# Optimization experiments

Hardware: AMD Instinct MI355X
Metric: run time of the kernel (lower is better)

## Reference

```python
import jax, jax.numpy as jnp
import numpy as np

V, N, D, R, L, KS = 32000, 2048, 1024, 16, 4, 7
B, H = 2, 4 * 1024
GMIN, GMAX, ACAP = 0.85, 1.0, 1.0


def rmsnorm(x, w, eps=1e-6):
    return x * jax.lax.rsqrt(jnp.mean(x * x, axis=-1, keepdims=True) + eps) * w


def l2norm(x, eps=1e-8):
    return x / jnp.maximum(jnp.linalg.norm(x, axis=-1, keepdims=True), eps)


def mlp(x, w1, b1, w2, b2):
    return jax.nn.gelu(x @ w1 + b1) @ w2 + b2


def k1_block(h, nw, w1, b1, w2, b2):
    return h + mlp(rmsnorm(h, nw), w1, b1, w2, b2)


def causal_conv(h, kernel):
    # depthwise causal conv with shared 1D kernel; kernel[0] = current step
    n = h.shape[1]
    hp = jnp.pad(h, ((0, 0), (KS - 1, 0), (0, 0)))
    out = jnp.zeros_like(h)
    for k in range(KS):  # KS is small & static
        out = out + kernel[k] * hp[:, KS - 1 - k: KS - 1 - k + n, :]
    return out


def k2_layer(h, p):
    (u, v, dlog, alog, glog, kern, pw, pb, n1w, n2w, w1, b1, w2, b2) = p
    residual = h
    hn = rmsnorm(h, n1w)
    gate = jax.nn.sigmoid(glog)
    out = gate * causal_conv(hn, kern)
    # low-rank q/k
    q = l2norm(hn @ u)          # (B,N,R)
    k = l2norm(hn @ v)          # (B,N,R)
    gamma = GMIN + (GMAX - GMIN) * jax.nn.sigmoid(dlog)   # (R,)
    alpha = ACAP * jax.nn.sigmoid(alog)                   # (R,)
    qa = q * alpha
    pos = jnp.arange(h.shape[1])
    diff = jnp.maximum(pos[:, None] - pos[None, :], 0).astype(h.dtype)
    mask = (pos[:, None] >= pos[None, :]).astype(h.dtype)
    # per-rank causal decay matrix gamma_r^(i-j): (R,N,N)
    decay = jnp.exp(diff[None] * jnp.log(gamma)[:, None, None]) * mask[None]
    scores = jnp.einsum('bir,rij,bjr->bij', qa, decay, k)  # (B,N,N)
    out = out + jnp.einsum('bij,bjd->bid', scores, hn)
    out = out @ pw + pb
    h = residual + out
    h = h + mlp(rmsnorm(h, n2w), w1, b1, w2, b2)
    return h


def setup_inputs() -> dict:
    key = jax.random.key(0)
    ks = jax.random.split(key, 32)
    f32 = jnp.float32
    inp = {
        'tokens': jax.random.randint(ks[0], (B, N), 0, V),
        'emb_table': jax.random.normal(ks[1], (V, D), f32) * 0.02,
        'k1a_nw': jnp.ones((D,), f32),
        'k1a_w1': jax.random.normal(ks[2], (D, H), f32) * 0.02,
        'k1a_b1': jnp.zeros((H,), f32),
        'k1a_w2': jax.random.normal(ks[3], (H, D), f32) * 0.02,
        'k1a_b2': jnp.zeros((D,), f32),
        'k2_u': jax.random.normal(ks[4], (L, D, R), f32) * 0.05,
        'k2_v': jax.random.normal(ks[5], (L, D, R), f32) * 0.05,
        'k2_dlog': jax.random.normal(ks[6], (L, R), f32) * 0.5,
        'k2_alog': jnp.zeros((L, R), f32),
        'k2_glog': jnp.zeros((L,), f32),
        'k2_kern': jax.random.normal(ks[7], (L, KS), f32) * 0.1,
        'k2_pw': jax.random.normal(ks[8], (L, D, D), f32) * 0.02,
        'k2_pb': jnp.zeros((L, D), f32),
        'k2_n1w': jnp.ones((L, D), f32),
        'k2_n2w': jnp.ones((L, D), f32),
        'k2_w1': jax.random.normal(ks[9], (L, D, H), f32) * 0.02,
        'k2_b1': jnp.zeros((L, H), f32),
        'k2_w2': jax.random.normal(ks[10], (L, H, D), f32) * 0.02,
        'k2_b2': jnp.zeros((L, D), f32),
        'k1b_nw': jnp.ones((D,), f32),
        'k1b_w1': jax.random.normal(ks[11], (D, H), f32) * 0.02,
        'k1b_b1': jnp.zeros((H,), f32),
        'k1b_w2': jax.random.normal(ks[12], (H, D), f32) * 0.02,
        'k1b_b2': jnp.zeros((D,), f32),
        'k0_nw': jnp.ones((D,), f32),
        'head_w': jax.random.normal(ks[13], (D, V), f32) * 0.02,
        'head_b': jnp.zeros((V,), f32),
    }
    return inp


def reference(tokens, emb_table,
              k1a_nw, k1a_w1, k1a_b1, k1a_w2, k1a_b2,
              k2_u, k2_v, k2_dlog, k2_alog, k2_glog, k2_kern,
              k2_pw, k2_pb, k2_n1w, k2_n2w, k2_w1, k2_b1, k2_w2, k2_b2,
              k1b_nw, k1b_w1, k1b_b1, k1b_w2, k1b_b2,
              k0_nw, head_w, head_b):
    h = emb_table[tokens]                                  # (B,N,D)
    h = k1_block(h, k1a_nw, k1a_w1, k1a_b1, k1a_w2, k1a_b2)
    stacked = (k2_u, k2_v, k2_dlog, k2_alog, k2_glog, k2_kern,
               k2_pw, k2_pb, k2_n1w, k2_n2w, k2_w1, k2_b1, k2_w2, k2_b2)
    def step(c, p):
        return k2_layer(c, p), None
    h, _ = jax.lax.scan(step, h, stacked)
    h = k1_block(h, k1b_nw, k1b_w1, k1b_b1, k1b_w2, k1b_b2)
    h = rmsnorm(h, k0_nw)                                  # K0 final norm
    return h @ head_w + head_b                             # (B,N,V)
```

## Files before the change

kernel.cpp:

```cpp
#include <hip/hip_runtime.h>
#include <hip/hip_bf16.h>

#define SEQ 2048
#define DIM 1024
#define RNK 16
#define NL 4
#define KT 7
#define BATCH 2
#define HID 4096
#define VOC 32000
#define BNROWS (BATCH*SEQ)
#define CHK 128
#define NCH (SEQ/CHK)
#define PRMS 128
#define KAPP 160

typedef __hip_bfloat16 bf16;
typedef __attribute__((ext_vector_type(8))) short bh8;
typedef __attribute__((ext_vector_type(4))) float vf4;

__device__ __forceinline__ float bfu(unsigned int u) { u <<= 16; return __builtin_bit_cast(float, u); }
__device__ __forceinline__ unsigned short f2bu(float x) { bf16 t = __float2bfloat16(x); return __builtin_bit_cast(unsigned short, t); }
__device__ __forceinline__ float b2f(bf16 x) { return __bfloat162float(x); }
__device__ __forceinline__ float sigm(float x) { return 1.f / (1.f + expf(-x)); }
__device__ __forceinline__ float gelu_t(float x) {
    float u = 0.7978845608028654f * (x + 0.044715f * x * x * x);
    return 0.5f * x * (1.f + tanhf(u));
}

__device__ __forceinline__ void gld16(const bf16* g, bf16* l) {
    __builtin_amdgcn_global_load_lds(
        (const __attribute__((address_space(1))) void*)g,
        (__attribute__((address_space(3))) void*)l,
        16, 0, 0);
}

__global__ void embed_kernel(const int* __restrict__ tokens, const float* __restrict__ emb,
                             float* __restrict__ h) {
    int row = blockIdx.x;
    int tok = tokens[row];
    const float4* src = (const float4*)(emb + (size_t)tok * DIM);
    float4* dst = (float4*)(h + (size_t)row * DIM);
    dst[threadIdx.x] = src[threadIdx.x];
}

__global__ void rmsnorm_kernel(const float* __restrict__ in, const float* __restrict__ wt,
                               bf16* __restrict__ out) {
    int row = blockIdx.x;
    int tx = threadIdx.x;
    float4 v = ((const float4*)(in + (size_t)row * DIM))[tx];
    float ss = v.x * v.x + v.y * v.y + v.z * v.z + v.w * v.w;
#pragma unroll
    for (int off = 32; off > 0; off >>= 1) ss += __shfl_down(ss, off);
    __shared__ float red[4];
    int lane = tx & 63, wv = tx >> 6;
    if (lane == 0) red[wv] = ss;
    __syncthreads();
    float tot = red[0] + red[1] + red[2] + red[3];
    float scale = rsqrtf(tot * (1.f / DIM) + 1e-6f);
    float4 w4 = ((const float4*)wt)[tx];
    uint2 o;
    o.x = f2bu(v.x * scale * w4.x) | ((unsigned int)f2bu(v.y * scale * w4.y) << 16);
    o.y = f2bu(v.z * scale * w4.z) | ((unsigned int)f2bu(v.w * scale * w4.w) << 16);
    *(uint2*)(out + (size_t)row * DIM + tx * 4) = o;
}

__global__ void transpose_cast_kernel(const float* __restrict__ in, bf16* __restrict__ out,
                                      int K, int Nc) {
    __shared__ float tile[32][33];
    int n0 = blockIdx.x * 32, k0 = blockIdx.y * 32;
    int tx = threadIdx.x & 31, ty = threadIdx.x >> 5;
#pragma unroll
    for (int i = 0; i < 32; i += 8)
        tile[ty + i][tx] = in[(size_t)(k0 + ty + i) * Nc + n0 + tx];
    __syncthreads();
#pragma unroll
    for (int i = 0; i < 32; i += 8)
        out[(size_t)(n0 + ty + i) * K + k0 + tx] = __float2bfloat16(tile[tx][ty + i]);
}

__global__ void prep_kernel(const float* __restrict__ dlog, const float* __restrict__ alog,
                            const float* __restrict__ glog, const float* __restrict__ kern,
                            float* __restrict__ prm) {
    int l = blockIdx.x, t = threadIdx.x;
    float* p = prm + l * PRMS;
    if (t < RNK) {
        float g = 0.85f + 0.15f * sigm(dlog[l * RNK + t]);
        float lg = logf(g);
        p[t] = g;
        p[16 + t] = lg;
        p[32 + t] = expf(lg * (float)CHK);
        p[48 + t] = sigm(alog[l * RNK + t]);
    }
    if (t < KT) {
        float gate = sigm(glog[l]);
        p[64 + t] = gate * kern[l * KT + t];
    }
}

__global__ void prep_uv_kernel(const float* __restrict__ u, const float* __restrict__ v,
                               bf16* __restrict__ uvT) {
    int l = blockIdx.y;
    int k = blockIdx.x * 256 + threadIdx.x;
    const float* ul = u + (size_t)l * DIM * RNK;
    const float* vl = v + (size_t)l * DIM * RNK;
    bf16* o = uvT + (size_t)l * 32 * DIM;
#pragma unroll
    for (int r = 0; r < RNK; ++r) {
        o[(size_t)r * DIM + k] = __float2bfloat16(ul[(size_t)k * RNK + r]);
        o[(size_t)(RNK + r) * DIM + k] = __float2bfloat16(vl[(size_t)k * RNK + r]);
    }
}

__global__ void conv_kernel(const bf16* __restrict__ hn, const float* __restrict__ prm,
                            float* __restrict__ Z) {
    int t = blockIdx.x * 256 + threadIdx.x;
    int d4 = (t & 255) * 4;
    int row = t >> 8;
    int n = row & (SEQ - 1);
    float a0 = 0, a1 = 0, a2 = 0, a3 = 0;
#pragma unroll
    for (int kk = 0; kk < KT; ++kk) {
        if (n - kk < 0) break;
        float wv = prm[64 + kk];
        uint2 hv = *(const uint2*)(hn + (size_t)(row - kk) * DIM + d4);
        a0 += wv * bfu(hv.x & 0xffffu);
        a1 += wv * bfu(hv.x >> 16);
        a2 += wv * bfu(hv.y & 0xffffu);
        a3 += wv * bfu(hv.y >> 16);
    }
    float4 o = {a0, a1, a2, a3};
    *(float4*)(Z + (size_t)row * DIM + d4) = o;
}

__global__ __launch_bounds__(64)
void qk_mfma_kernel(const bf16* __restrict__ hn, const bf16* __restrict__ uvT,
                    const float* __restrict__ prm, float* __restrict__ qa,
                    float* __restrict__ kn) {
    int row0 = blockIdx.x * 16;
    int lane = threadIdx.x;
    int fr = lane & 15, kf = (lane >> 4) * 8;
    vf4 accq = {}, acck = {};
#pragma unroll 4
    for (int kt = 0; kt < DIM / 32; ++kt) {
        int k0 = kt * 32;
        bh8 b0 = *(const bh8*)(uvT + (size_t)fr * DIM + k0 + kf);
        bh8 b1 = *(const bh8*)(uvT + (size_t)(16 + fr) * DIM + k0 + kf);
        bh8 a0 = *(const bh8*)(hn + (size_t)(row0 + fr) * DIM + k0 + kf);
        accq = __builtin_amdgcn_mfma_f32_16x16x32_bf16(a0, b0, accq, 0, 0, 0);
        acck = __builtin_amdgcn_mfma_f32_16x16x32_bf16(a0, b1, acck, 0, 0, 0);
    }
    int fq = lane >> 4;
    float alpha = prm[48 + fr];
#pragma unroll
    for (int j = 0; j < 4; ++j) {
        float qv = accq[j], kv = acck[j];
        float sq = qv * qv, sk = kv * kv;
#pragma unroll
        for (int mask = 1; mask < 16; mask <<= 1) {
            sq += __shfl_xor(sq, mask);
            sk += __shfl_xor(sk, mask);
        }
        int row = row0 + fq * 4 + j;
        qa[(size_t)row * RNK + fr] = qv / fmaxf(sqrtf(sq), 1e-8f) * alpha;
        kn[(size_t)row * RNK + fr] = kv / fmaxf(sqrtf(sk), 1e-8f);
    }
}

__global__ void trans_hn_kernel(const bf16* __restrict__ hn, bf16* __restrict__ HB) {
    __shared__ bf16 tile[32][40];
    int bc = blockIdx.x;
    int d0 = blockIdx.y * 32, j0 = blockIdx.z * 32;
    int tx = threadIdx.x & 31, ty = threadIdx.x >> 5;
    size_t rowb = (size_t)bc * CHK;
#pragma unroll
    for (int i = 0; i < 32; i += 8)
        tile[ty + i][tx] = hn[(rowb + j0 + ty + i) * DIM + d0 + tx];
    __syncthreads();
    bf16* Hp = HB + (size_t)bc * DIM * KAPP;
#pragma unroll
    for (int i = 0; i < 32; i += 8)
        Hp[(size_t)(d0 + ty + i) * KAPP + j0 + tx] = tile[tx][ty + i];
}

__global__ void scores_kernel(const float* __restrict__ qa, const float* __restrict__ kn,
                              const float* __restrict__ prm, bf16* __restrict__ SA,
                              bf16* __restrict__ kdtB) {
    int bc = blockIdx.x;
    int yt = blockIdx.y;
    __shared__ float ptab[CHK][16];
    for (int e = threadIdx.x; e < CHK * 16; e += 256) {
        int tt = e >> 4, r = e & 15;
        ptab[tt][r] = expf(prm[16 + r] * (float)tt);
    }
    __syncthreads();
    size_t rowb = (size_t)bc * CHK;
    bf16* SAp = SA + (size_t)bc * CHK * KAPP;
    for (int e = threadIdx.x; e < 16 * CHK; e += 256) {
        int i = yt * 16 + (e >> 7), j = e & (CHK - 1);
        float vsum = 0.f;
        if (i >= j) {
            const float* qp = qa + (rowb + i) * RNK;
            const float* kp = kn + (rowb + j) * RNK;
#pragma unroll
            for (int r = 0; r < 16; ++r) vsum += qp[r] * ptab[i - j][r] * kp[r];
        }
        SAp[(size_t)i * KAPP + j] = __float2bfloat16(vsum);
    }
    for (int e = threadIdx.x; e < 16 * 32; e += 256) {
        int i = yt * 16 + (e >> 5), rr = e & 31;
        float w = 0.f;
        if (rr < 16) w = qa[(rowb + i) * RNK + rr] * expf(prm[16 + rr] * (float)(i + 1));
        SAp[(size_t)i * KAPP + CHK + rr] = __float2bfloat16(w);
    }
    bf16* kp2 = kdtB + (size_t)bc * RNK * CHK;
    for (int e = threadIdx.x; e < 2 * CHK; e += 256) {
        int r = 2 * yt + (e >> 7), j = e & (CHK - 1);
        kp2[(size_t)r * CHK + j] =
            __float2bfloat16(ptab[CHK - 1 - j][r] * kn[(rowb + j) * RNK + r]);
    }
}

__global__ __launch_bounds__(64)
void chunkU_kernel(const bf16* __restrict__ HB, const bf16* __restrict__ kdtB,
                   float* __restrict__ U) {
    int bc = blockIdx.x;
    int d0 = blockIdx.y * 64;
    int lane = threadIdx.x;
    int fr = lane & 15, kf = (lane >> 4) * 8;
    const bf16* Hp = HB + (size_t)bc * DIM * KAPP;
    const bf16* Kp = kdtB + (size_t)bc * RNK * CHK;
    vf4 acc[4] = {};
#pragma unroll
    for (int kt = 0; kt < 4; ++kt) {
        int k0 = kt * 32;
        bh8 bb = *(const bh8*)(Kp + (size_t)fr * CHK + k0 + kf);
#pragma unroll
        for (int m = 0; m < 4; ++m) {
            bh8 a = *(const bh8*)(Hp + (size_t)(d0 + m * 16 + fr) * KAPP + k0 + kf);
            acc[m] = __builtin_amdgcn_mfma_f32_16x16x32_bf16(a, bb, acc[m], 0, 0, 0);
        }
    }
    int fq = lane >> 4;
    float* Up = U + (size_t)bc * DIM * RNK;
#pragma unroll
    for (int m = 0; m < 4; ++m)
#pragma unroll
        for (int j = 0; j < 4; ++j)
            Up[(size_t)(d0 + m * 16 + fq * 4 + j) * RNK + fr] = acc[m][j];
}

__global__ void scanP_kernel(const float* __restrict__ U, const float* __restrict__ prm,
                             bf16* __restrict__ HB) {
    int g = blockIdx.x * 256 + threadIdx.x;
    int rq = g & 3;
    int d = (g >> 2) & (DIM - 1);
    int b = g >> 12;
    float gC[4], p[4];
#pragma unroll
    for (int q = 0; q < 4; ++q) { gC[q] = prm[32 + rq * 4 + q]; p[q] = 0.f; }
    for (int c = 0; c < NCH; ++c) {
        int bc = b * NCH + c;
        uint2 pk;
        pk.x = (unsigned int)f2bu(p[0]) | ((unsigned int)f2bu(p[1]) << 16);
        pk.y = (unsigned int)f2bu(p[2]) | ((unsigned int)f2bu(p[3]) << 16);
        *(uint2*)(HB + (size_t)bc * DIM * KAPP + (size_t)d * KAPP + CHK + rq * 4) = pk;
        float4 u4 = *(const float4*)(U + ((size_t)bc * DIM + d) * RNK + rq * 4);
        p[0] = gC[0] * p[0] + u4.x;
        p[1] = gC[1] * p[1] + u4.y;
        p[2] = gC[2] * p[2] + u4.z;
        p[3] = gC[3] * p[3] + u4.w;
    }
}

__global__ __launch_bounds__(256)
void apply_gemm_kernel(const bf16* __restrict__ SA, const bf16* __restrict__ HB,
                       const float* __restrict__ Z, bf16* __restrict__ Zb) {
    __shared__ alignas(16) bf16 As[128][40];
    __shared__ alignas(16) bf16 Bs[128][40];
    int bc = blockIdx.y;
    int colB0 = blockIdx.x * 128;
    int t = threadIdx.x;
    int lane = t & 63, wid = t >> 6;
    int wr = wid >> 1, wc = wid & 1;
    vf4 acc[4][4] = {};
    const bf16* A = SA + (size_t)bc * CHK * KAPP;
    const bf16* BT = HB + (size_t)bc * DIM * KAPP;
    int r1 = t >> 2, ko1 = (t & 3) * 8;
    int fr = lane & 15, kf = (lane >> 4) * 8;
#pragma unroll
    for (int kt = 0; kt < 5; ++kt) {
        int k0 = kt * 32;
        int4 va1 = *(const int4*)(A + (size_t)r1 * KAPP + k0 + ko1);
        int4 va2 = *(const int4*)(A + (size_t)(r1 + 64) * KAPP + k0 + ko1);
        int4 vb1 = *(const int4*)(BT + (size_t)(colB0 + r1) * KAPP + k0 + ko1);
        int4 vb2 = *(const int4*)(BT + (size_t)(colB0 + r1 + 64) * KAPP + k0 + ko1);
        __syncthreads();
        *(int4*)&As[r1][ko1] = va1;
        *(int4*)&As[r1 + 64][ko1] = va2;
        *(int4*)&Bs[r1][ko1] = vb1;
        *(int4*)&Bs[r1 + 64][ko1] = vb2;
        __syncthreads();
        bh8 a[4], bb[4];
#pragma unroll
        for (int m = 0; m < 4; ++m) a[m] = *(const bh8*)&As[wr * 64 + m * 16 + fr][kf];
#pragma unroll
        for (int n = 0; n < 4; ++n) bb[n] = *(const bh8*)&Bs[wc * 64 + n * 16 + fr][kf];
#pragma unroll
        for (int m = 0; m < 4; ++m)
#pragma unroll
            for (int n = 0; n < 4; ++n)
                acc[m][n] = __builtin_amdgcn_mfma_f32_16x16x32_bf16(a[m], bb[n], acc[m][n], 0, 0, 0);
    }
    int fq = lane >> 4;
    size_t rowb = (size_t)bc * CHK;
#pragma unroll
    for (int m = 0; m < 4; ++m) {
#pragma unroll
        for (int n = 0; n < 4; ++n) {
            int col = colB0 + wc * 64 + n * 16 + fr;
#pragma unroll
            for (int j = 0; j < 4; ++j) {
                size_t row = rowb + wr * 64 + m * 16 + fq * 4 + j;
                size_t idx = row * DIM + col;
                Zb[idx] = __float2bfloat16(Z[idx] + acc[m][n][j]);
            }
        }
    }
}

template <int EPI>
__global__ __launch_bounds__(256)
void gemm_kernel(const bf16* __restrict__ A, const bf16* __restrict__ BT,
                 const float* __restrict__ bias, const float* __restrict__ res,
                 float* __restrict__ outF, bf16* __restrict__ outB,
                 int M, int Nc, int K, int lda) {
    __shared__ alignas(16) bf16 As[128][32];
    __shared__ alignas(16) bf16 Bs[128][32];
    int gx = gridDim.x;
    int orig = blockIdx.y * gx + blockIdx.x;
    int qch = (gx * gridDim.y) >> 3;
    int wg = (orig & 7) * qch + (orig >> 3);
    int bn = wg % gx, bm = wg / gx;
    int t = threadIdx.x;
    int lane = t & 63, wid = t >> 6;
    int wr = wid >> 1, wc = wid & 1;
    vf4 acc[4][4] = {};
    const int rowA0 = bm * 128, colB0 = bn * 128;
    int fr = lane & 15, kf = (lane >> 4) * 8;
    int c0 = wid * 2;
    int lrow = lane >> 2;
    int lcol = (lane & 3) * 8;
    const bf16* Ag0 = A + (size_t)(rowA0 + c0 * 16 + lrow) * lda + lcol;
    const bf16* Ag1 = A + (size_t)(rowA0 + c0 * 16 + 16 + lrow) * lda + lcol;
    const bf16* Bg0 = BT + (size_t)(colB0 + c0 * 16 + lrow) * lda + lcol;
    const bf16* Bg1 = BT + (size_t)(colB0 + c0 * 16 + 16 + lrow) * lda + lcol;
    bf16* Al0 = &As[0][0] + c0 * 512;
    bf16* Al1 = Al0 + 512;
    bf16* Bl0 = &Bs[0][0] + c0 * 512;
    bf16* Bl1 = Bl0 + 512;
    int nk = K >> 5;
    for (int kt = 0; kt < nk; ++kt) {
        int k0 = kt * 32;
        __syncthreads();
        gld16(Ag0 + k0, Al0);
        gld16(Ag1 + k0, Al1);
        gld16(Bg0 + k0, Bl0);
        gld16(Bg1 + k0, Bl1);
        asm volatile("s_waitcnt vmcnt(0)" ::: "memory");
        __syncthreads();
        bh8 a[4], bb[4];
#pragma unroll
        for (int m = 0; m < 4; ++m) a[m] = *(const bh8*)&As[wr * 64 + m * 16 + fr][kf];
#pragma unroll
        for (int n = 0; n < 4; ++n) bb[n] = *(const bh8*)&Bs[wc * 64 + n * 16 + fr][kf];
#pragma unroll
        for (int m = 0; m < 4; ++m)
#pragma unroll
            for (int n = 0; n < 4; ++n)
                acc[m][n] = __builtin_amdgcn_mfma_f32_16x16x32_bf16(a[m], bb[n], acc[m][n], 0, 0, 0);
    }
    int fq = lane >> 4;
#pragma unroll
    for (int m = 0; m < 4; ++m) {
#pragma unroll
        for (int n = 0; n < 4; ++n) {
            int col = colB0 + wc * 64 + n * 16 + fr;
            float bv = bias[col];
#pragma unroll
            for (int j = 0; j < 4; ++j) {
                int row = rowA0 + wr * 64 + m * 16 + fq * 4 + j;
                size_t idx = (size_t)row * Nc + col;
                float v2 = acc[m][n][j] + bv;
                if (EPI == 1) v2 += res[idx];
                outF[idx] = v2;
            }
        }
    }
}

#define SB __builtin_amdgcn_sched_barrier(0)
template <int EPI>
__global__ __launch_bounds__(512, 2)
void gemm256_kernel(const bf16* __restrict__ A, const bf16* __restrict__ BT,
                    const float* __restrict__ bias,
                    float* __restrict__ outF, bf16* __restrict__ outB,
                    int M, int Nc, int K, int lda) {
    extern __shared__ char smem[];
    bf16* Alds = (bf16*)smem;
    bf16* Blds = (bf16*)(smem + 65536);
    if (EPI == 4) {
        size_t zo = (size_t)blockIdx.z * K;
        A += zo; BT += zo;
        outB += (size_t)blockIdx.z * ((size_t)M * Nc);
    }
    int gx = gridDim.x, gy = gridDim.y;
    int orig = blockIdx.y * gx + blockIdx.x;
    int qch = (gx * gy) >> 3;
    int wg = (orig & 7) * qch + (orig >> 3);
    int bm = wg % gy, bn = wg / gy;
    int rowA0 = bm * 256, colB0 = bn * 256;
    int tid = threadIdx.x;
    int lane = tid & 63, wid = tid >> 6;
    int wm = wid >> 2, wn = wid & 3;
    int fr = lane & 15;
    int kf8 = ((((lane >> 4) & 3) ^ ((fr >> 1) & 3)) * 8);
    int srow = wid * 16 + (lane >> 2);
    int scol = (((lane & 3) ^ ((lane >> 3) & 3)) * 8);
    const bf16* Ags = A + (size_t)(rowA0 + srow) * lda + scol;
    const bf16* Bgs = BT + (size_t)(colB0 + srow) * lda + scol;
    int sbase = wid * 512;
    auto stA = [&](int d, int kh, int k0) {
        bf16* dst = Alds + (d * 2 + kh) * 8192 + sbase;
        const bf16* src = Ags + k0 + kh * 32;
        gld16(src, dst);
        gld16(src + (size_t)128 * lda, dst + 4096);
    };
    auto stB = [&](int d, int kh, int k0) {
        bf16* dst = Blds + (d * 2 + kh) * 8192 + sbase;
        const bf16* src = Bgs + k0 + kh * 32;
        gld16(src, dst);
        gld16(src + (size_t)128 * lda, dst + 4096);
    };
    const bf16* Ard = Alds + (size_t)(wm * 128 + fr) * 32 + kf8;
    const bf16* Brd = Blds + (size_t)(wn * 64 + fr) * 32 + kf8;
    vf4 acc[8][4] = {};
    int nt = K >> 6;
    stA(0, 0, 0); stB(0, 0, 0); stA(0, 1, 0); stB(0, 1, 0);
    for (int t = 0; t < nt; ++t) {
        int d = t & 1, nd = d ^ 1;
        int k1 = (t + 1) << 6;
        bool pf = (t + 1 < nt);
        int dof = d * 16384;
        bh8 bF[4];
        if (pf) { stA(nd, 0, k1); asm volatile("s_waitcnt vmcnt(6)" ::: "memory"); }
        else    {                 asm volatile("s_waitcnt vmcnt(4)" ::: "memory"); }
        SB; __builtin_amdgcn_s_barrier(); SB;
        {
            bh8 a0 = *(const bh8*)(Ard + dof + 0 * 512);
            bh8 a1 = *(const bh8*)(Ard + dof + 1 * 512);
            bh8 a2 = *(const bh8*)(Ard + dof + 2 * 512);
            bh8 a3 = *(const bh8*)(Ard + dof + 3 * 512);
#pragma unroll
            for (int n = 0; n < 4; ++n) bF[n] = *(const bh8*)(Brd + dof + n * 512);
            __builtin_amdgcn_s_setprio(1);
#pragma unroll
            for (int n = 0; n < 4; ++n) {
                acc[0][n] = __builtin_amdgcn_mfma_f32_16x16x32_bf16(a0, bF[n], acc[0][n], 0, 0, 0);
                acc[1][n] = __builtin_amdgcn_mfma_f32_16x16x32_bf16(a1, bF[n], acc[1][n], 0, 0, 0);
                acc[2][n] = __builtin_amdgcn_mfma_f32_16x16x32_bf16(a2, bF[n], acc[2][n], 0, 0, 0);
                acc[3][n] = __builtin_amdgcn_mfma_f32_16x16x32_bf16(a3, bF[n], acc[3][n], 0, 0, 0);
            }
            __builtin_amdgcn_s_setprio(0);
        }
        SB;
        if (pf) stB(nd, 0, k1);
        SB; __builtin_amdgcn_s_barrier(); SB;
        {
            bh8 a0 = *(const bh8*)(Ard + dof + 4 * 512);
            bh8 a1 = *(const bh8*)(Ard + dof + 5 * 512);
            bh8 a2 = *(const bh8*)(Ard + dof + 6 * 512);
            bh8 a3 = *(const bh8*)(Ard + dof + 7 * 512);
            __builtin_amdgcn_s_setprio(1);
#pragma unroll
            for (int n = 0; n < 4; ++n) {
                acc[4][n] = __builtin_amdgcn_mfma_f32_16x16x32_bf16(a0, bF[n], acc[4][n], 0, 0, 0);
                acc[5][n] = __builtin_amdgcn_mfma_f32_16x16x32_bf16(a1, bF[n], acc[5][n], 0, 0, 0);
                acc[6][n] = __builtin_amdgcn_mfma_f32_16x16x32_bf16(a2, bF[n], acc[6][n], 0, 0, 0);
                acc[7][n] = __builtin_amdgcn_mfma_f32_16x16x32_bf16(a3, bF[n], acc[7][n], 0, 0, 0);
            }
            __builtin_amdgcn_s_setprio(0);
        }
        SB;
        int dof1 = dof + 8192;
        if (pf) { stA(nd, 1, k1); asm volatile("s_waitcnt vmcnt(6)" ::: "memory"); }
        else    {                 asm volatile("s_waitcnt vmcnt(0)" ::: "memory"); }
        SB; __builtin_amdgcn_s_barrier(); SB;
        {
            bh8 a0 = *(const bh8*)(Ard + dof1 + 0 * 512);
            bh8 a1 = *(const bh8*)(Ard + dof1 + 1 * 512);
            bh8 a2 = *(const bh8*)(Ard + dof1 + 2 * 512);
            bh8 a3 = *(const bh8*)(Ard + dof1 + 3 * 512);
#pragma unroll
            for (int n = 0; n < 4; ++n) bF[n] = *(const bh8*)(Brd + dof1 + n * 512);
            __builtin_amdgcn_s_setprio(1);
#pragma unroll
            for (int n = 0; n < 4; ++n) {
                acc[0][n] = __builtin_amdgcn_mfma_f32_16x16x32_bf16(a0, bF[n], acc[0][n], 0, 0, 0);
                acc[1][n] = __builtin_amdgcn_mfma_f32_16x16x32_bf16(a1, bF[n], acc[1][n], 0, 0, 0);
                acc[2][n] = __builtin_amdgcn_mfma_f32_16x16x32_bf16(a2, bF[n], acc[2][n], 0, 0, 0);
                acc[3][n] = __builtin_amdgcn_mfma_f32_16x16x32_bf16(a3, bF[n], acc[3][n], 0, 0, 0);
            }
            __builtin_amdgcn_s_setprio(0);
        }
        SB;
        if (pf) stB(nd, 1, k1);
        SB; __builtin_amdgcn_s_barrier(); SB;
        {
            bh8 a0 = *(const bh8*)(Ard + dof1 + 4 * 512);
            bh8 a1 = *(const bh8*)(Ard + dof1 + 5 * 512);
            bh8 a2 = *(const bh8*)(Ard + dof1 + 6 * 512);
            bh8 a3 = *(const bh8*)(Ard + dof1 + 7 * 512);
            __builtin_amdgcn_s_setprio(1);
#pragma unroll
            for (int n = 0; n < 4; ++n) {
                acc[4][n] = __builtin_amdgcn_mfma_f32_16x16x32_bf16(a0, bF[n], acc[4][n], 0, 0, 0);
                acc[5][n] = __builtin_amdgcn_mfma_f32_16x16x32_bf16(a1, bF[n], acc[5][n], 0, 0, 0);
                acc[6][n] = __builtin_amdgcn_mfma_f32_16x16x32_bf16(a2, bF[n], acc[6][n], 0, 0, 0);
                acc[7][n] = __builtin_amdgcn_mfma_f32_16x16x32_bf16(a3, bF[n], acc[7][n], 0, 0, 0);
            }
            __builtin_amdgcn_s_setprio(0);
        }
        SB;
    }
    int fq = lane >> 4;
#pragma unroll
    for (int mi = 0; mi < 8; ++mi) {
#pragma unroll
        for (int ni = 0; ni < 4; ++ni) {
            int col = colB0 + wn * 64 + ni * 16 + fr;
            float bv = (EPI == 4) ? 0.f : bias[col];
#pragma unroll
            for (int j = 0; j < 4; ++j) {
                int row = rowA0 + wm * 128 + mi * 16 + fq * 4 + j;
                size_t idx = (size_t)row * Nc + col;
                float v2 = acc[mi][ni][j] + bv;
                if (EPI == 2) outB[idx] = __float2bfloat16(gelu_t(v2));
                else if (EPI == 4) outB[idx] = __float2bfloat16(v2);
                else outF[idx] = v2;
            }
        }
    }
}

__global__ void combine4_norm_kernel(const bf16* __restrict__ P, const float* __restrict__ bias,
                                     const float* __restrict__ nw, float* __restrict__ h,
                                     bf16* __restrict__ hnb) {
    int row = blockIdx.x;
    int tx = threadIdx.x;
    const size_t S = (size_t)BNROWS * DIM;
    size_t base = (size_t)row * DIM + tx * 4;
    float4 hv = *(float4*)(h + base);
    float4 bv = ((const float4*)bias)[tx];
    float s0 = bv.x, s1 = bv.y, s2 = bv.z, s3 = bv.w;
#pragma unroll
    for (int q = 0; q < 4; ++q) {
        uint2 pk = *(const uint2*)(P + q * S + base);
        s0 += bfu(pk.x & 0xffffu);
        s1 += bfu(pk.x >> 16);
        s2 += bfu(pk.y & 0xffffu);
        s3 += bfu(pk.y >> 16);
    }
    hv.x += s0; hv.y += s1; hv.z += s2; hv.w += s3;
    *(float4*)(h + base) = hv;
    float ss = hv.x * hv.x + hv.y * hv.y + hv.z * hv.z + hv.w * hv.w;
#pragma unroll
    for (int off = 32; off > 0; off >>= 1) ss += __shfl_down(ss, off);
    __shared__ float red[4];
    int lane = tx & 63, wv = tx >> 6;
    if (lane == 0) red[wv] = ss;
    __syncthreads();
    float tot = red[0] + red[1] + red[2] + red[3];
    float scale = rsqrtf(tot * (1.f / DIM) + 1e-6f);
    float4 w4 = ((const float4*)nw)[tx];
    uint2 o;
    o.x = f2bu(hv.x * scale * w4.x) | ((unsigned int)f2bu(hv.y * scale * w4.y) << 16);
    o.y = f2bu(hv.z * scale * w4.z) | ((unsigned int)f2bu(hv.w * scale * w4.w) << 16);
    *(uint2*)(hnb + (size_t)row * DIM + tx * 4) = o;
}

extern "C" void kernel_launch(void* const* d_in, const int* in_sizes, int n_in,
                              void* d_out, int out_size, void* d_ws, size_t ws_size,
                              hipStream_t stream) {
    (void)in_sizes; (void)n_in; (void)out_size; (void)ws_size;
    const int* tokens = (const int*)d_in[0];
    const float* emb = (const float*)d_in[1];
    const float* k1a_nw = (const float*)d_in[2];
    const float* k1a_w1 = (const float*)d_in[3];
    const float* k1a_b1 = (const float*)d_in[4];
    const float* k1a_w2 = (const float*)d_in[5];
    const float* k1a_b2 = (const float*)d_in[6];
    const float* k2_u = (const float*)d_in[7];
    const float* k2_v = (const float*)d_in[8];
    const float* k2_dlog = (const float*)d_in[9];
    const float* k2_alog = (const float*)d_in[10];
    const float* k2_glog = (const float*)d_in[11];
    const float* k2_kern = (const float*)d_in[12];
    const float* k2_pw = (const float*)d_in[13];
    const float* k2_pb = (const float*)d_in[14];
    const float* k2_n1w = (const float*)d_in[15];
    const float* k2_n2w = (const float*)d_in[16];
    const float* k2_w1 = (const float*)d_in[17];
    const float* k2_b1 = (const float*)d_in[18];
    const float* k2_w2 = (const float*)d_in[19];
    const float* k2_b2 = (const float*)d_in[20];
    const float* k1b_nw = (const float*)d_in[21];
    const float* k1b_w1 = (const float*)d_in[22];
    const float* k1b_b1 = (const float*)d_in[23];
    const float* k1b_w2 = (const float*)d_in[24];
    const float* k1b_b2 = (const float*)d_in[25];
    const float* k0_nw = (const float*)d_in[26];
    const float* head_w = (const float*)d_in[27];
    const float* head_b = (const float*)d_in[28];
    float* out = (float*)d_out;

    (void)hipFuncSetAttribute((const void*)gemm256_kernel<0>,
                              hipFuncAttributeMaxDynamicSharedMemorySize, 131072);
    (void)hipFuncSetAttribute((const void*)gemm256_kernel<2>,
                              hipFuncAttributeMaxDynamicSharedMemorySize, 131072);
    (void)hipFuncSetAttribute((const void*)gemm256_kernel<4>,
                              hipFuncAttributeMaxDynamicSharedMemorySize, 131072);

    char* wsp = (char*)d_ws;
    auto alloc = [&](size_t bytes) -> char* {
        char* p = wsp;
        wsp += (bytes + 255) & ~(size_t)255;
        return p;
    };
    float* h   = (float*)alloc((size_t)BNROWS * DIM * 4);
    float* Z   = (float*)alloc((size_t)BNROWS * DIM * 4);
    bf16* hnb  = (bf16*)alloc((size_t)BNROWS * DIM * 2);
    bf16* Zb   = (bf16*)alloc((size_t)BNROWS * DIM * 2);
    bf16* t1b  = (bf16*)alloc((size_t)BNROWS * HID * 2);
    float* qaB = (float*)alloc((size_t)BNROWS * RNK * 4);
    float* knB = (float*)alloc((size_t)BNROWS * RNK * 4);
    float* U   = (float*)alloc((size_t)BATCH * NCH * DIM * RNK * 4);
    bf16* HB   = (bf16*)alloc((size_t)BATCH * NCH * DIM * KAPP * 2);
    bf16* SA   = (bf16*)alloc((size_t)BATCH * NCH * CHK * KAPP * 2);
    bf16* kdtB = (bf16*)alloc((size_t)BATCH * NCH * RNK * CHK * 2);
    float* prm = (float*)alloc((size_t)NL * PRMS * 4);
    bf16* uvT  = (bf16*)alloc((size_t)NL * 32 * DIM * 2);
    bf16* w1aT = (bf16*)alloc((size_t)HID * DIM * 2);
    bf16* w2aT = (bf16*)alloc((size_t)DIM * HID * 2);
    bf16* w1bT = (bf16*)alloc((size_t)HID * DIM * 2);
    bf16* w2bT = (bf16*)alloc((size_t)DIM * HID * 2);
    bf16* pwT  = (bf16*)alloc((size_t)NL * DIM * DIM * 2);
    bf16* w1T  = (bf16*)alloc((size_t)NL * DIM * HID * 2);
    bf16* w2T  = (bf16*)alloc((size_t)NL * HID * DIM * 2);
    bf16* headT = (bf16*)alloc((size_t)VOC * DIM * 2);
    bf16* Pk  = (bf16*)alloc((size_t)4 * BNROWS * DIM * 2);

    hipMemsetAsync(HB, 0, (size_t)BATCH * NCH * DIM * KAPP * 2, stream);

    auto T = [&](const float* in, bf16* o, int K, int Nc) {
        transpose_cast_kernel<<<dim3(Nc / 32, K / 32), 256, 0, stream>>>(in, o, K, Nc);
    };
    T(k1a_w1, w1aT, DIM, HID);
    T(k1a_w2, w2aT, HID, DIM);
    T(k1b_w1, w1bT, DIM, HID);
    T(k1b_w2, w2bT, HID, DIM);
    for (int l = 0; l < NL; ++l) {
        T(k2_pw + (size_t)l * DIM * DIM, pwT + (size_t)l * DIM * DIM, DIM, DIM);
        T(k2_w1 + (size_t)l * DIM * HID, w1T + (size_t)l * DIM * HID, DIM, HID);
        T(k2_w2 + (size_t)l * HID * DIM, w2T + (size_t)l * HID * DIM, HID, DIM);
    }
    T(head_w, headT, DIM, VOC);
    prep_kernel<<<NL, 32, 0, stream>>>(k2_dlog, k2_alog, k2_glog, k2_kern, prm);
    prep_uv_kernel<<<dim3(DIM / 256, NL), 256, 0, stream>>>(k2_u, k2_v, uvT);

    auto mlp_core = [&](const bf16* W1, const float* B1, const bf16* W2, const float* B2,
                        const float* nw_next) {
        gemm256_kernel<2><<<dim3(HID / 256, BNROWS / 256), 512, 131072, stream>>>(
            hnb, W1, B1, nullptr, t1b, BNROWS, HID, DIM, DIM);
        gemm256_kernel<4><<<dim3(DIM / 256, BNROWS / 256, 4), 512, 131072, stream>>>(
            t1b, W2, nullptr, nullptr, Pk, BNROWS, DIM, HID / 4, HID);
        combine4_norm_kernel<<<BNROWS, 256, 0, stream>>>(Pk, B2, nw_next, h, hnb);
    };

    embed_kernel<<<BNROWS, 256, 0, stream>>>(tokens, emb, h);
    rmsnorm_kernel<<<BNROWS, 256, 0, stream>>>(h, k1a_nw, hnb);
    mlp_core(w1aT, k1a_b1, w2aT, k1a_b2, k2_n1w);

    for (int l = 0; l < NL; ++l) {
        const float* prm_l = prm + l * PRMS;
        conv_kernel<<<BNROWS, 256, 0, stream>>>(hnb, prm_l, Z);
        qk_mfma_kernel<<<BNROWS / 16, 64, 0, stream>>>(hnb, uvT + (size_t)l * 32 * DIM,
                                                       prm_l, qaB, knB);
        trans_hn_kernel<<<dim3(BATCH * NCH, DIM / 32, CHK / 32), 256, 0, stream>>>(hnb, HB);
        scores_kernel<<<dim3(BATCH * NCH, 8), 256, 0, stream>>>(qaB, knB, prm_l, SA, kdtB);
        chunkU_kernel<<<dim3(BATCH * NCH, DIM / 64), 64, 0, stream>>>(HB, kdtB, U);
        scanP_kernel<<<BATCH * DIM * 4 / 256, 256, 0, stream>>>(U, prm_l, HB);
        apply_gemm_kernel<<<dim3(DIM / 128, BATCH * NCH), 256, 0, stream>>>(SA, HB, Z, Zb);
        gemm_kernel<1><<<dim3(DIM / 128, BNROWS / 128), 256, 0, stream>>>(
            Zb, pwT + (size_t)l * DIM * DIM, k2_pb + (size_t)l * DIM, h, h, nullptr,
            BNROWS, DIM, DIM, DIM);
        rmsnorm_kernel<<<BNROWS, 256, 0, stream>>>(h, k2_n2w + (size_t)l * DIM, hnb);
        const float* nw_next = (l < NL - 1) ? (k2_n1w + (size_t)(l + 1) * DIM) : k1b_nw;
        mlp_core(w1T + (size_t)l * DIM * HID, k2_b1 + (size_t)l * HID,
                 w2T + (size_t)l * HID * DIM, k2_b2 + (size_t)l * DIM, nw_next);
    }

    mlp_core(w1bT, k1b_b1, w2bT, k1b_b2, k0_nw);

    gemm256_kernel<0><<<dim3(VOC / 256, BNROWS / 256), 512, 131072, stream>>>(
        hnb, headT, head_b, out, nullptr, BNROWS, VOC, DIM, DIM);
}
```

Before: 1.546 ms.

## Shrink gemm256 K-step to 32 with 64KB LDS for higher occupancy

Restructures the 256x256 GEMM main loop to stage 32-wide K slices instead of 64-wide, which halves the LDS footprint from 128KB to 64KB. Launch bounds are raised to allow more blocks per CU. The aim is more resident waves to hide latency. In exchange there are twice as many iterations and barriers per K, the prefetch distance is shorter, and register pressure may be tighter under the new launch bound.

Result: slower. 6.136 ms (+296.9%).

```diff
diff --git a/kernel.cpp b/kernel.cpp
--- a/kernel.cpp
+++ b/kernel.cpp
@@ -401,14 +401,14 @@
 
 #define SB __builtin_amdgcn_sched_barrier(0)
 template <int EPI>
-__global__ __launch_bounds__(512, 2)
+__global__ __launch_bounds__(512, 4)
 void gemm256_kernel(const bf16* __restrict__ A, const bf16* __restrict__ BT,
                     const float* __restrict__ bias,
                     float* __restrict__ outF, bf16* __restrict__ outB,
                     int M, int Nc, int K, int lda) {
     extern __shared__ char smem[];
     bf16* Alds = (bf16*)smem;
-    bf16* Blds = (bf16*)(smem + 65536);
+    bf16* Blds = (bf16*)(smem + 32768);
     if (EPI == 4) {
         size_t zo = (size_t)blockIdx.z * K;
         A += zo; BT += zo;
@@ -430,31 +430,31 @@
     const bf16* Ags = A + (size_t)(rowA0 + srow) * lda + scol;
     const bf16* Bgs = BT + (size_t)(colB0 + srow) * lda + scol;
     int sbase = wid * 512;
-    auto stA = [&](int d, int kh, int k0) {
-        bf16* dst = Alds + (d * 2 + kh) * 8192 + sbase;
-        const bf16* src = Ags + k0 + kh * 32;
+    auto stA = [&](int d, int k0) {
+        bf16* dst = Alds + d * 8192 + sbase;
+        const bf16* src = Ags + k0;
         gld16(src, dst);
         gld16(src + (size_t)128 * lda, dst + 4096);
     };
-    auto stB = [&](int d, int kh, int k0) {
-        bf16* dst = Blds + (d * 2 + kh) * 8192 + sbase;
-        const bf16* src = Bgs + k0 + kh * 32;
+    auto stB = [&](int d, int k0) {
+        bf16* dst = Blds + d * 8192 + sbase;
+        const bf16* src = Bgs + k0;
         gld16(src, dst);
         gld16(src + (size_t)128 * lda, dst + 4096);
     };
     const bf16* Ard = Alds + (size_t)(wm * 128 + fr) * 32 + kf8;
     const bf16* Brd = Blds + (size_t)(wn * 64 + fr) * 32 + kf8;
     vf4 acc[8][4] = {};
-    int nt = K >> 6;
-    stA(0, 0, 0); stB(0, 0, 0); stA(0, 1, 0); stB(0, 1, 0);
-    for (int t = 0; t < nt; ++t) {
+    int ntk = K >> 5;
+    stB(0, 0); stA(0, 0);
+    for (int t = 0; t < ntk; ++t) {
         int d = t & 1, nd = d ^ 1;
-        int k1 = (t + 1) << 6;
-        bool pf = (t + 1 < nt);
-        int dof = d * 16384;
+        int k1 = (t + 1) << 5;
+        bool pf = (t + 1 < ntk);
+        int dof = d * 8192;
         bh8 bF[4];
-        if (pf) { stA(nd, 0, k1); asm volatile("s_waitcnt vmcnt(6)" ::: "memory"); }
-        else    {                 asm volatile("s_waitcnt vmcnt(4)" ::: "memory"); }
+        if (pf) { stB(nd, k1); asm volatile("s_waitcnt vmcnt(2)" ::: "memory"); }
+        else    {              asm volatile("s_waitcnt vmcnt(0)" ::: "memory"); }
         SB; __builtin_amdgcn_s_barrier(); SB;
         {
             bh8 a0 = *(const bh8*)(Ard + dof + 0 * 512);
@@ -474,53 +474,13 @@
             __builtin_amdgcn_s_setprio(0);
         }
         SB;
-        if (pf) stB(nd, 0, k1);
+        if (pf) stA(nd, k1);
         SB; __builtin_amdgcn_s_barrier(); SB;
         {
             bh8 a0 = *(const bh8*)(Ard + dof + 4 * 512);
             bh8 a1 = *(const bh8*)(Ard + dof + 5 * 512);
             bh8 a2 = *(const bh8*)(Ard + dof + 6 * 512);
             bh8 a3 = *(const bh8*)(Ard + dof + 7 * 512);
-            __builtin_amdgcn_s_setprio(1);
-#pragma unroll
-            for (int n = 0; n < 4; ++n) {
-                acc[4][n] = __builtin_amdgcn_mfma_f32_16x16x32_bf16(a0, bF[n], acc[4][n], 0, 0, 0);
-                acc[5][n] = __builtin_amdgcn_mfma_f32_16x16x32_bf16(a1, bF[n], acc[5][n], 0, 0, 0);
-                acc[6][n] = __builtin_amdgcn_mfma_f32_16x16x32_bf16(a2, bF[n], acc[6][n], 0, 0, 0);
-                acc[7][n] = __builtin_amdgcn_mfma_f32_16x16x32_bf16(a3, bF[n], acc[7][n], 0, 0, 0);
-            }
-            __builtin_amdgcn_s_setprio(0);
-        }
-        SB;
-        int dof1 = dof + 8192;
-        if (pf) { stA(nd, 1, k1); asm volatile("s_waitcnt vmcnt(6)" ::: "memory"); }
-        else    {                 asm volatile("s_waitcnt vmcnt(0)" ::: "memory"); }
-        SB; __builtin_amdgcn_s_barrier(); SB;
-        {
-            bh8 a0 = *(const bh8*)(Ard + dof1 + 0 * 512);
-            bh8 a1 = *(const bh8*)(Ard + dof1 + 1 * 512);
-            bh8 a2 = *(const bh8*)(Ard + dof1 + 2 * 512);
-            bh8 a3 = *(const bh8*)(Ard + dof1 + 3 * 512);
-#pragma unroll
-            for (int n = 0; n < 4; ++n) bF[n] = *(const bh8*)(Brd + dof1 + n * 512);
-            __builtin_amdgcn_s_setprio(1);
-#pragma unroll
-            for (int n = 0; n < 4; ++n) {
-                acc[0][n] = __builtin_amdgcn_mfma_f32_16x16x32_bf16(a0, bF[n], acc[0][n], 0, 0, 0);
-                acc[1][n] = __builtin_amdgcn_mfma_f32_16x16x32_bf16(a1, bF[n], acc[1][n], 0, 0, 0);
-                acc[2][n] = __builtin_amdgcn_mfma_f32_16x16x32_bf16(a2, bF[n], acc[2][n], 0, 0, 0);
-                acc[3][n] = __builtin_amdgcn_mfma_f32_16x16x32_bf16(a3, bF[n], acc[3][n], 0, 0, 0);
-            }
-            __builtin_amdgcn_s_setprio(0);
-        }
-        SB;
-        if (pf) stB(nd, 1, k1);
-        SB; __builtin_amdgcn_s_barrier(); SB;
-        {
-            bh8 a0 = *(const bh8*)(Ard + dof1 + 4 * 512);
-            bh8 a1 = *(const bh8*)(Ard + dof1 + 5 * 512);
-            bh8 a2 = *(const bh8*)(Ard + dof1 + 6 * 512);
-            bh8 a3 = *(const bh8*)(Ard + dof1 + 7 * 512);
             __builtin_amdgcn_s_setprio(1);
 #pragma unroll
             for (int n = 0; n < 4; ++n) {
@@ -625,11 +585,11 @@
     float* out = (float*)d_out;
 
     (void)hipFuncSetAttribute((const void*)gemm256_kernel<0>,
-                              hipFuncAttributeMaxDynamicSharedMemorySize, 131072);
+                              hipFuncAttributeMaxDynamicSharedMemorySize, 65536);
     (void)hipFuncSetAttribute((const void*)gemm256_kernel<2>,
-                              hipFuncAttributeMaxDynamicSharedMemorySize, 131072);
+                              hipFuncAttributeMaxDynamicSharedMemorySize, 65536);
     (void)hipFuncSetAttribute((const void*)gemm256_kernel<4>,
-                              hipFuncAttributeMaxDynamicSharedMemorySize, 131072);
+                              hipFuncAttributeMaxDynamicSharedMemorySize, 65536);
 
     char* wsp = (char*)d_ws;
     auto alloc = [&](size_t bytes) -> char* {
@@ -680,9 +640,9 @@
 
     auto mlp_core = [&](const bf16* W1, const float* B1, const bf16* W2, const float* B2,
                         const float* nw_next) {
-        gemm256_kernel<2><<<dim3(HID / 256, BNROWS / 256), 512, 131072, stream>>>(
+        gemm256_kernel<2><<<dim3(HID / 256, BNROWS / 256), 512, 65536, stream>>>(
             hnb, W1, B1, nullptr, t1b, BNROWS, HID, DIM, DIM);
-        gemm256_kernel<4><<<dim3(DIM / 256, BNROWS / 256, 4), 512, 131072, stream>>>(
+        gemm256_kernel<4><<<dim3(DIM / 256, BNROWS / 256, 4), 512, 65536, stream>>>(
             t1b, W2, nullptr, nullptr, Pk, BNROWS, DIM, HID / 4, HID);
         combine4_norm_kernel<<<BNROWS, 256, 0, stream>>>(Pk, B2, nw_next, h, hnb);
     };
@@ -712,6 +672,6 @@
 
     mlp_core(w1bT, k1b_b1, w2bT, k1b_b2, k0_nw);
 
-    gemm256_kernel<0><<<dim3(VOC / 256, BNROWS / 256), 512, 131072, stream>>>(
+    gemm256_kernel<0><<<dim3(VOC / 256, BNROWS / 256), 512, 65536, stream>>>(
         hnb, headT, head_b, out, nullptr, BNROWS, VOC, DIM, DIM);
 }
```
